# Optimization experiments

Measured on AMD Instinct MI355X. Metric: run time of the kernel, lower is better.

The kernel has to match this reference:

```python
import jax, jax.numpy as jnp
import numpy as np

N, K, D, H = 8192, 32, 128, 256

def setup_inputs() -> dict:
    key = jax.random.key(0)
    ks = jax.random.split(key, 12)
    x = jax.random.normal(ks[0], (N, D), dtype=jnp.float32)
    chosen = jax.random.randint(ks[1], (N, K), 0, N, dtype=jnp.int32)
    # column 0 = the node's own index (matches neighbors[0] == current in the torch code)
    nbrs = jnp.concatenate([jnp.arange(N, dtype=jnp.int32)[:, None], chosen], axis=1)
    t = jax.random.normal(ks[2], (N,), dtype=jnp.float32)
    e_hat = jax.random.normal(ks[3], (N,), dtype=jnp.float32)
    def lin(k, fan_in, fan_out):
        k1, k2 = jax.random.split(k)
        s = 1.0 / np.sqrt(fan_in)
        W = jax.random.uniform(k1, (fan_in, fan_out), minval=-s, maxval=s, dtype=jnp.float32)
        bb = jax.random.uniform(k2, (fan_out,), minval=-s, maxval=s, dtype=jnp.float32)
        return W, bb
    W1, b1 = lin(ks[4], 2 * D, H)
    W2, b2 = lin(ks[5], H, H)
    W3, b3 = lin(ks[6], H, 1)
    b = jnp.float32(1.0)
    return {"x": x, "nbrs": nbrs, "t": t, "e_hat": e_hat,
            "W1": W1, "b1": b1, "W2": W2, "b2": b2, "W3": W3, "b3": b3, "b": b}

def reference(x, nbrs, t, e_hat, W1, b1, W2, b2, W3, b3, b):
    n, d = x.shape
    cur = nbrs[:, 0]          # [n] node's own index
    chosen = nbrs[:, 1:]      # [n, K] neighbor indices
    k = chosen.shape[1]
    z_i = x[cur]              # [n, d]
    z_j = x[chosen]           # [n, K, d] ragged gather (regular degree)
    z_concat = jnp.concatenate(
        [jnp.broadcast_to(z_i[:, None, :], (n, k, d)), z_j], axis=-1)  # [n, K, 2d]
    h = jax.nn.relu(z_concat @ W1 + b1)
    h = jax.nn.relu(h @ W2 + b2)
    mlp_neigh = (h @ W3 + b3)[..., 0]                     # [n, K]
    scores = jax.nn.softmax(b * jnp.abs(mlp_neigh), axis=1)  # per-node softmax
    prop_res = t[chosen] - e_hat[chosen]                  # [n, K]
    w = mlp_neigh * scores                                # [n, K]
    Y_pred = jnp.sum(prop_res * w, axis=1)                # [n]
    pairwise = jnp.zeros((n, n), dtype=x.dtype).at[cur[:, None], chosen].set(w)
    pairwise = pairwise.at[cur, cur].set(0.0)             # zero self-weight last, as in torch
    return Y_pred, pairwise
```

## Files before the change

kernel.cpp:

```cpp
#include <hip/hip_runtime.h>
#include <hip/hip_bf16.h>

typedef short s8v __attribute__((ext_vector_type(8)));
typedef float f4v __attribute__((ext_vector_type(4)));
typedef float f2v __attribute__((ext_vector_type(2)));
typedef unsigned u4v __attribute__((ext_vector_type(4)));

#define NN 8192
#define KN 32
#define DD 128
#define HH 256

static __device__ __forceinline__ unsigned short f2bf(float f) {
    union { float f; unsigned u; } v; v.f = f;
    unsigned r = v.u + 0x7fffu + ((v.u >> 16) & 1u);
    return (unsigned short)(r >> 16);
}
static __device__ __forceinline__ float bf2f(unsigned short h) {
    union { unsigned u; float f; } v; v.u = ((unsigned)h) << 16;
    return v.f;
}
static __device__ __forceinline__ unsigned cvt2(float a, float b) {
    float2 f2; f2.x = a; f2.y = b;
    __hip_bfloat162 h = __float22bfloat162_rn(f2);
    union { __hip_bfloat162 h; unsigned u; } c; c.h = h;
    return c.u;
}
static __device__ __forceinline__ f2v unpk2(unsigned qd) {
    union { unsigned u; float f; } lo, hi;
    lo.u = qd << 16; hi.u = qd & 0xffff0000u;
    f2v r; r[0] = lo.f; r[1] = hi.f; return r;
}

__global__ __launch_bounds__(256) void prep_kernel(
    const float* __restrict__ W1, const float* __restrict__ W2,
    unsigned short* __restrict__ W1sh, unsigned short* __restrict__ W1sl,
    unsigned short* __restrict__ W2s)
{
    int tid = blockIdx.x * 256 + threadIdx.x;
    if (tid < 128 * 512) {
        int k = tid >> 9;
        int n = tid & 511;
        float w = (n < 256) ? W1[k * 256 + n] : W1[(128 + k) * 256 + (n - 256)];
        unsigned short hi = f2bf(w);
        float lo = w - bf2f(hi);
        int idx = ((k >> 5) * 512 + n) * 32 + (k & 31);
        W1sh[idx] = hi;
        W1sl[idx] = f2bf(lo);
    } else {
        int t2 = tid - 128 * 512;
        int k = t2 >> 8;
        int n = t2 & 255;
        W2s[((k >> 5) * 256 + n) * 32 + (k & 31)] = f2bf(W2[k * 256 + n]);
    }
}

__global__ __launch_bounds__(256) void pq_kernel(
    const float* __restrict__ x, const unsigned short* __restrict__ W1sh,
    const unsigned short* __restrict__ W1sl, const float* __restrict__ b1,
    float* __restrict__ P, unsigned short* __restrict__ Q)
{
    __shared__ unsigned short Ah[64 * 136];
    __shared__ unsigned short Al[64 * 136];
    int t  = threadIdx.x;
    int r0 = blockIdx.x * 64;
    int n0 = blockIdx.y * 256;

    {
        int m   = (t & 15) | ((t >> 6) << 4);
        int seg = (t >> 4) & 3;
        const float* xr = x + (r0 + m) * DD + seg * 32;
        #pragma unroll
        for (int it = 0; it < 4; ++it) {
            f4v v0 = *(const f4v*)(xr + it * 8);
            f4v v1 = *(const f4v*)(xr + it * 8 + 4);
            u4v hh, ll;
            #pragma unroll
            for (int pp = 0; pp < 4; ++pp) {
                f2v v;
                v[0] = (pp < 2) ? v0[pp * 2]     : v1[(pp - 2) * 2];
                v[1] = (pp < 2) ? v0[pp * 2 + 1] : v1[(pp - 2) * 2 + 1];
                unsigned hd = cvt2(v[0], v[1]);
                f2v hf = unpk2(hd);
                f2v lo = v - hf;
                hh[pp] = hd;
                ll[pp] = cvt2(lo[0], lo[1]);
            }
            int c = seg * 32 + it * 8;
            *(u4v*)(Ah + m * 136 + c) = hh;
            *(u4v*)(Al + m * 136 + c) = ll;
        }
    }
    __syncthreads();

    int lane = t & 63, wn = t >> 6, l15 = lane & 15, q = lane >> 4;
    f4v acc[4][4];
    #pragma unroll
    for (int mt = 0; mt < 4; ++mt)
        #pragma unroll
        for (int nt = 0; nt < 4; ++nt) acc[mt][nt] = (f4v){0.f, 0.f, 0.f, 0.f};

    #pragma unroll
    for (int kt = 0; kt < 4; ++kt) {
        s8v ah[4], al[4], bh[4], bl[4];
        #pragma unroll
        for (int mt = 0; mt < 4; ++mt) {
            int m = mt * 16 + l15;
            ah[mt] = *(const s8v*)(Ah + m * 136 + kt * 32 + q * 8);
            al[mt] = *(const s8v*)(Al + m * 136 + kt * 32 + q * 8);
        }
        #pragma unroll
        for (int nt = 0; nt < 4; ++nt) {
            int n = n0 + wn * 64 + nt * 16 + l15;
            int idx = (kt * 512 + n) * 32 + q * 8;
            bh[nt] = *(const s8v*)(W1sh + idx);
            bl[nt] = *(const s8v*)(W1sl + idx);
        }
        #pragma unroll
        for (int mt = 0; mt < 4; ++mt)
            #pragma unroll
            for (int nt = 0; nt < 4; ++nt) {
                acc[mt][nt] = __builtin_amdgcn_mfma_f32_16x16x32_bf16(ah[mt], bh[nt], acc[mt][nt], 0, 0, 0);
                acc[mt][nt] = __builtin_amdgcn_mfma_f32_16x16x32_bf16(ah[mt], bl[nt], acc[mt][nt], 0, 0, 0);
                acc[mt][nt] = __builtin_amdgcn_mfma_f32_16x16x32_bf16(al[mt], bh[nt], acc[mt][nt], 0, 0, 0);
            }
    }

    #pragma unroll
    for (int nt = 0; nt < 4; ++nt) {
        int cg = n0 + wn * 64 + nt * 16 + l15;
        if (cg < 256) {
            float bias = b1[cg];
            #pragma unroll
            for (int mt = 0; mt < 4; ++mt)
                #pragma unroll
                for (int r = 0; r < 4; ++r) {
                    int row = r0 + mt * 16 + q * 4 + r;
                    P[row * 256 + cg] = acc[mt][nt][r] + bias;
                }
        } else {
            int cq = cg - 256;
            #pragma unroll
            for (int mt = 0; mt < 4; ++mt)
                #pragma unroll
                for (int r = 0; r < 4; ++r) {
                    int row = r0 + mt * 16 + q * 4 + r;
                    Q[row * 256 + cq] = f2bf(acc[mt][nt][r]);
                }
        }
    }
}

__global__ __launch_bounds__(256) void main_kernel(
    const float* __restrict__ P, const unsigned short* __restrict__ Q,
    const unsigned short* __restrict__ W2s,
    const float* __restrict__ b2, const float* __restrict__ W3,
    const int* __restrict__ nbrs, const float* __restrict__ t_arr,
    const float* __restrict__ e_hat, const float* __restrict__ b3p,
    const float* __restrict__ bscal, float* __restrict__ out)
{
    __shared__ unsigned short A[64 * 264];
    __shared__ float mlpbuf[64][4];
    __shared__ float wbuf_w[2][32];
    __shared__ int   wbuf_j[2][32];
    int t = threadIdx.x;
    int node0 = blockIdx.x * 2;
    float* PW = out + NN;

    {
        int m   = (t & 15) | ((t >> 6) << 4);
        int seg = (t >> 4) & 3;
        int g = node0 + (m >> 5);
        int j = nbrs[g * 33 + 1 + (m & 31)];
        const float* Pr = P + g * 256 + seg * 64;
        const unsigned short* Qr = Q + j * 256 + seg * 64;

        #pragma unroll
        for (int half = 0; half < 2; ++half) {
            f4v p0[4], p1[4];
            u4v qv[4];
            #pragma unroll
            for (int it = 0; it < 4; ++it) {
                int itg = half * 4 + it;
                p0[it] = *(const f4v*)(Pr + itg * 8);
                p1[it] = *(const f4v*)(Pr + itg * 8 + 4);
                qv[it] = *(const u4v*)(Qr + itg * 8);
            }
            #pragma unroll
            for (int it = 0; it < 4; ++it) {
                int itg = half * 4 + it;
                u4v hv;
                #pragma unroll
                for (int pp = 0; pp < 4; ++pp) {
                    f2v pv;
                    pv[0] = (pp < 2) ? p0[it][pp * 2]     : p1[it][(pp - 2) * 2];
                    pv[1] = (pp < 2) ? p0[it][pp * 2 + 1] : p1[it][(pp - 2) * 2 + 1];
                    f2v qf = unpk2(qv[it][pp]);
                    f2v s = pv + qf;
                    s = __builtin_elementwise_max(s, (f2v){0.f, 0.f});
                    hv[pp] = cvt2(s[0], s[1]);
                }
                *(u4v*)(A + m * 264 + seg * 64 + itg * 8) = hv;
            }
        }
    }
    __syncthreads();

    int lane = t & 63, wn = t >> 6, l15 = lane & 15, q = lane >> 4;
    f4v acc[4][4];
    #pragma unroll
    for (int mt = 0; mt < 4; ++mt)
        #pragma unroll
        for (int nt = 0; nt < 4; ++nt) acc[mt][nt] = (f4v){0.f, 0.f, 0.f, 0.f};

    #pragma unroll
    for (int kt = 0; kt < 8; ++kt) {
        s8v a[4], b[4];
        #pragma unroll
        for (int mt = 0; mt < 4; ++mt)
            a[mt] = *(const s8v*)(A + (mt * 16 + l15) * 264 + kt * 32 + q * 8);
        #pragma unroll
        for (int nt = 0; nt < 4; ++nt) {
            int n = wn * 64 + nt * 16 + l15;
            b[nt] = *(const s8v*)(W2s + (kt * 256 + n) * 32 + q * 8);
        }
        #pragma unroll
        for (int mt = 0; mt < 4; ++mt)
            #pragma unroll
            for (int nt = 0; nt < 4; ++nt)
                acc[mt][nt] = __builtin_amdgcn_mfma_f32_16x16x32_bf16(a[mt], b[nt], acc[mt][nt], 0, 0, 0);
    }

    f2v p2[4][2];
    #pragma unroll
    for (int mt = 0; mt < 4; ++mt) {
        p2[mt][0] = (f2v){0.f, 0.f};
        p2[mt][1] = (f2v){0.f, 0.f};
    }
    #pragma unroll
    for (int nt = 0; nt < 4; ++nt) {
        int c = wn * 64 + nt * 16 + l15;
        float bb = b2[c], w3 = W3[c];
        f2v bb2 = (f2v){bb, bb};
        f2v w32 = (f2v){w3, w3};
        #pragma unroll
        for (int mt = 0; mt < 4; ++mt) {
            f2v lo = (f2v){acc[mt][nt][0], acc[mt][nt][1]};
            f2v hi = (f2v){acc[mt][nt][2], acc[mt][nt][3]};
            lo = lo + bb2;
            hi = hi + bb2;
            lo = __builtin_elementwise_max(lo, (f2v){0.f, 0.f});
            hi = __builtin_elementwise_max(hi, (f2v){0.f, 0.f});
            p2[mt][0] = p2[mt][0] + lo * w32;
            p2[mt][1] = p2[mt][1] + hi * w32;
        }
    }
    #pragma unroll
    for (int off = 1; off < 16; off <<= 1)
        #pragma unroll
        for (int mt = 0; mt < 4; ++mt)
            #pragma unroll
            for (int rr = 0; rr < 2; ++rr)
                #pragma unroll
                for (int cc = 0; cc < 2; ++cc)
                    p2[mt][rr][cc] += __shfl_xor(p2[mt][rr][cc], off, 64);
    if (l15 == 0) {
        #pragma unroll
        for (int mt = 0; mt < 4; ++mt)
            #pragma unroll
            for (int r = 0; r < 4; ++r)
                mlpbuf[mt * 16 + q * 4 + r][wn] = p2[mt][r >> 1][r & 1];
    }
    __syncthreads();

    float* img = (float*)A;
    if (t < 128) {
        int node = t >> 6;
        int k = t & 63;
        if (k < 32) {
            int g = node0 + node;
            int m = node * 32 + k;
            float mlp = mlpbuf[m][0] + mlpbuf[m][1] + mlpbuf[m][2] + mlpbuf[m][3] + b3p[0];
            float aabs = bscal[0] * fabsf(mlp);
            float amax = aabs;
            #pragma unroll
            for (int off = 1; off < 32; off <<= 1)
                amax = fmaxf(amax, __shfl_xor(amax, off, 64));
            float e = __expf(aabs - amax);
            float s = e;
            #pragma unroll
            for (int off = 1; off < 32; off <<= 1)
                s += __shfl_xor(s, off, 64);
            float w = mlp * (e / s);

            int j = nbrs[g * 33 + 1 + k];
            float prop = t_arr[j] - e_hat[j];
            float yp = prop * w;
            #pragma unroll
            for (int off = 1; off < 32; off <<= 1)
                yp += __shfl_xor(yp, off, 64);
            if (k == 0) out[g] = yp;

            bool write = (j != g);
            for (int kk = 0; kk < 32; ++kk) {
                int jv = __shfl(j, kk, 64);
                if (kk > k && jv == j) write = false;
            }
            wbuf_w[node][k] = w;
            wbuf_j[node][k] = write ? j : -1;
        }
    } else {
        int tt = t - 128;
        f4v z = (f4v){0.f, 0.f, 0.f, 0.f};
        #pragma unroll
        for (int i = 0; i < 16; ++i)
            *(f4v*)(img + tt * 4 + i * 512) = z;
    }
    __syncthreads();

    if (t < 32) {
        int j = wbuf_j[0][t];
        if (j >= 0) img[j] = wbuf_w[0][t];
    }
    __syncthreads();
    {
        float* dst = PW + (long)node0 * NN;
        f4v z = (f4v){0.f, 0.f, 0.f, 0.f};
        #pragma unroll
        for (int i = 0; i < 8; ++i) {
            f4v v = *(const f4v*)(img + t * 4 + i * 1024);
            *(f4v*)(img + t * 4 + i * 1024) = z;
            __builtin_nontemporal_store(v, (f4v*)(dst + t * 4 + i * 1024));
        }
    }
    __syncthreads();
    if (t < 32) {
        int j = wbuf_j[1][t];
        if (j >= 0) img[j] = wbuf_w[1][t];
    }
    __syncthreads();
    {
        float* dst = PW + (long)(node0 + 1) * NN;
        #pragma unroll
        for (int i = 0; i < 8; ++i) {
            f4v v = *(const f4v*)(img + t * 4 + i * 1024);
            __builtin_nontemporal_store(v, (f4v*)(dst + t * 4 + i * 1024));
        }
    }
}

extern "C" void kernel_launch(void* const* d_in, const int* in_sizes, int n_in,
                              void* d_out, int out_size, void* d_ws, size_t ws_size,
                              hipStream_t stream) {
    const float* x     = (const float*)d_in[0];
    const int*   nbrs  = (const int*)d_in[1];
    const float* t     = (const float*)d_in[2];
    const float* e_hat = (const float*)d_in[3];
    const float* W1    = (const float*)d_in[4];
    const float* b1    = (const float*)d_in[5];
    const float* W2    = (const float*)d_in[6];
    const float* b2    = (const float*)d_in[7];
    const float* W3    = (const float*)d_in[8];
    const float* b3    = (const float*)d_in[9];
    const float* b     = (const float*)d_in[10];

    char* ws = (char*)d_ws;
    float*          P     = (float*)ws;
    unsigned short* Q     = (unsigned short*)(ws + 8388608);
    unsigned short* W1sh  = (unsigned short*)(ws + 12582912);
    unsigned short* W1sl  = (unsigned short*)(ws + 12713984);
    unsigned short* W2s   = (unsigned short*)(ws + 12845056);

    prep_kernel<<<512, 256, 0, stream>>>(W1, W2, W1sh, W1sl, W2s);
    pq_kernel<<<dim3(128, 2), 256, 0, stream>>>(x, W1sh, W1sl, b1, P, Q);
    main_kernel<<<4096, 256, 0, stream>>>(P, Q, W2s, b2, W3, nbrs, t, e_hat,
                                          b3, b, (float*)d_out);
}
```

Baseline: 351.6 us.

## Process one node per 128-thread block instead of two per 256-thread block

Restructures main_kernel so each block handles a single node with 2 waves, each wave computing a 32x128 MFMA tile, and the pairwise row is written in two 4096-column halves through a smaller LDS image. The grid doubles to 8192 blocks and the LDS footprint halves, aiming for more resident blocks and finer-grained scheduling. In exchange, each W2 tile load is shared across fewer rows (32 instead of 64), so W2 traffic per node roughly doubles, and each wave holds more B fragments.

```diff
diff --git a/kernel.cpp b/kernel.cpp
--- a/kernel.cpp
+++ b/kernel.cpp
@@ -151,7 +151,7 @@
     }
 }
 
-__global__ __launch_bounds__(256) void main_kernel(
+__global__ __launch_bounds__(128, 4) void main_kernel(
     const float* __restrict__ P, const unsigned short* __restrict__ Q,
     const unsigned short* __restrict__ W2s,
     const float* __restrict__ b2, const float* __restrict__ W3,
@@ -159,92 +159,80 @@
     const float* __restrict__ e_hat, const float* __restrict__ b3p,
     const float* __restrict__ bscal, float* __restrict__ out)
 {
-    __shared__ unsigned short A[64 * 264];
-    __shared__ float mlpbuf[64][4];
-    __shared__ float wbuf_w[2][32];
-    __shared__ int   wbuf_j[2][32];
+    __shared__ unsigned short A[32 * 264];
+    __shared__ float mlpbuf[32][2];
+    __shared__ float wbuf_w[32];
+    __shared__ int   wbuf_j[32];
     int t = threadIdx.x;
-    int node0 = blockIdx.x * 2;
+    int g = blockIdx.x;
     float* PW = out + NN;
 
     {
         int m   = (t & 15) | ((t >> 6) << 4);
         int seg = (t >> 4) & 3;
-        int g = node0 + (m >> 5);
-        int j = nbrs[g * 33 + 1 + (m & 31)];
+        int j = nbrs[g * 33 + 1 + m];
         const float* Pr = P + g * 256 + seg * 64;
         const unsigned short* Qr = Q + j * 256 + seg * 64;
-
-        #pragma unroll
-        for (int half = 0; half < 2; ++half) {
-            f4v p0[4], p1[4];
-            u4v qv[4];
-            #pragma unroll
-            for (int it = 0; it < 4; ++it) {
-                int itg = half * 4 + it;
-                p0[it] = *(const f4v*)(Pr + itg * 8);
-                p1[it] = *(const f4v*)(Pr + itg * 8 + 4);
-                qv[it] = *(const u4v*)(Qr + itg * 8);
+        #pragma unroll
+        for (int it = 0; it < 8; ++it) {
+            f4v p0 = *(const f4v*)(Pr + it * 8);
+            f4v p1 = *(const f4v*)(Pr + it * 8 + 4);
+            u4v qv = *(const u4v*)(Qr + it * 8);
+            u4v hv;
+            #pragma unroll
+            for (int pp = 0; pp < 4; ++pp) {
+                f2v pv;
+                pv[0] = (pp < 2) ? p0[pp * 2]     : p1[(pp - 2) * 2];
+                pv[1] = (pp < 2) ? p0[pp * 2 + 1] : p1[(pp - 2) * 2 + 1];
+                f2v qf = unpk2(qv[pp]);
+                f2v s = pv + qf;
+                s = __builtin_elementwise_max(s, (f2v){0.f, 0.f});
+                hv[pp] = cvt2(s[0], s[1]);
             }
-            #pragma unroll
-            for (int it = 0; it < 4; ++it) {
-                int itg = half * 4 + it;
-                u4v hv;
-                #pragma unroll
-                for (int pp = 0; pp < 4; ++pp) {
-                    f2v pv;
-                    pv[0] = (pp < 2) ? p0[it][pp * 2]     : p1[it][(pp - 2) * 2];
-                    pv[1] = (pp < 2) ? p0[it][pp * 2 + 1] : p1[it][(pp - 2) * 2 + 1];
-                    f2v qf = unpk2(qv[it][pp]);
-                    f2v s = pv + qf;
-                    s = __builtin_elementwise_max(s, (f2v){0.f, 0.f});
-                    hv[pp] = cvt2(s[0], s[1]);
-                }
-                *(u4v*)(A + m * 264 + seg * 64 + itg * 8) = hv;
-            }
-        }
-    }
-    __syncthreads();
-
-    int lane = t & 63, wn = t >> 6, l15 = lane & 15, q = lane >> 4;
-    f4v acc[4][4];
-    #pragma unroll
-    for (int mt = 0; mt < 4; ++mt)
-        #pragma unroll
-        for (int nt = 0; nt < 4; ++nt) acc[mt][nt] = (f4v){0.f, 0.f, 0.f, 0.f};
+            *(u4v*)(A + m * 264 + seg * 64 + it * 8) = hv;
+        }
+    }
+    __syncthreads();
+
+    int lane = t & 63, w = t >> 6, l15 = lane & 15, q = lane >> 4;
+    f4v acc[2][8];
+    #pragma unroll
+    for (int mt = 0; mt < 2; ++mt)
+        #pragma unroll
+        for (int nt = 0; nt < 8; ++nt) acc[mt][nt] = (f4v){0.f, 0.f, 0.f, 0.f};
 
     #pragma unroll
     for (int kt = 0; kt < 8; ++kt) {
-        s8v a[4], b[4];
-        #pragma unroll
-        for (int mt = 0; mt < 4; ++mt)
+        s8v a[2], b[8];
+        #pragma unroll
+        for (int mt = 0; mt < 2; ++mt)
             a[mt] = *(const s8v*)(A + (mt * 16 + l15) * 264 + kt * 32 + q * 8);
         #pragma unroll
-        for (int nt = 0; nt < 4; ++nt) {
-            int n = wn * 64 + nt * 16 + l15;
+        for (int nt = 0; nt < 8; ++nt) {
+            int n = w * 128 + nt * 16 + l15;
             b[nt] = *(const s8v*)(W2s + (kt * 256 + n) * 32 + q * 8);
         }
         #pragma unroll
-        for (int mt = 0; mt < 4; ++mt)
-            #pragma unroll
-            for (int nt = 0; nt < 4; ++nt)
+        for (int mt = 0; mt < 2; ++mt)
+            #pragma unroll
+            for (int nt = 0; nt < 8; ++nt)
                 acc[mt][nt] = __builtin_amdgcn_mfma_f32_16x16x32_bf16(a[mt], b[nt], acc[mt][nt], 0, 0, 0);
     }
 
-    f2v p2[4][2];
-    #pragma unroll
-    for (int mt = 0; mt < 4; ++mt) {
+    f2v p2[2][2];
+    #pragma unroll
+    for (int mt = 0; mt < 2; ++mt) {
         p2[mt][0] = (f2v){0.f, 0.f};
         p2[mt][1] = (f2v){0.f, 0.f};
     }
     #pragma unroll
-    for (int nt = 0; nt < 4; ++nt) {
-        int c = wn * 64 + nt * 16 + l15;
+    for (int nt = 0; nt < 8; ++nt) {
+        int c = w * 128 + nt * 16 + l15;
         float bb = b2[c], w3 = W3[c];
         f2v bb2 = (f2v){bb, bb};
         f2v w32 = (f2v){w3, w3};
         #pragma unroll
-        for (int mt = 0; mt < 4; ++mt) {
+        for (int mt = 0; mt < 2; ++mt) {
             f2v lo = (f2v){acc[mt][nt][0], acc[mt][nt][1]};
             f2v hi = (f2v){acc[mt][nt][2], acc[mt][nt][3]};
             lo = lo + bb2;
@@ -258,7 +246,7 @@
     #pragma unroll
     for (int off = 1; off < 16; off <<= 1)
         #pragma unroll
-        for (int mt = 0; mt < 4; ++mt)
+        for (int mt = 0; mt < 2; ++mt)
             #pragma unroll
             for (int rr = 0; rr < 2; ++rr)
                 #pragma unroll
@@ -266,85 +254,80 @@
                     p2[mt][rr][cc] += __shfl_xor(p2[mt][rr][cc], off, 64);
     if (l15 == 0) {
         #pragma unroll
-        for (int mt = 0; mt < 4; ++mt)
+        for (int mt = 0; mt < 2; ++mt)
             #pragma unroll
             for (int r = 0; r < 4; ++r)
-                mlpbuf[mt * 16 + q * 4 + r][wn] = p2[mt][r >> 1][r & 1];
+                mlpbuf[mt * 16 + q * 4 + r][w] = p2[mt][r >> 1][r & 1];
     }
     __syncthreads();
 
     float* img = (float*)A;
-    if (t < 128) {
-        int node = t >> 6;
-        int k = t & 63;
-        if (k < 32) {
-            int g = node0 + node;
-            int m = node * 32 + k;
-            float mlp = mlpbuf[m][0] + mlpbuf[m][1] + mlpbuf[m][2] + mlpbuf[m][3] + b3p[0];
-            float aabs = bscal[0] * fabsf(mlp);
-            float amax = aabs;
-            #pragma unroll
-            for (int off = 1; off < 32; off <<= 1)
-                amax = fmaxf(amax, __shfl_xor(amax, off, 64));
-            float e = __expf(aabs - amax);
-            float s = e;
-            #pragma unroll
-            for (int off = 1; off < 32; off <<= 1)
-                s += __shfl_xor(s, off, 64);
-            float w = mlp * (e / s);
-
-            int j = nbrs[g * 33 + 1 + k];
-            float prop = t_arr[j] - e_hat[j];
-            float yp = prop * w;
-            #pragma unroll
-            for (int off = 1; off < 32; off <<= 1)
-                yp += __shfl_xor(yp, off, 64);
-            if (k == 0) out[g] = yp;
-
-            bool write = (j != g);
-            for (int kk = 0; kk < 32; ++kk) {
-                int jv = __shfl(j, kk, 64);
-                if (kk > k && jv == j) write = false;
-            }
-            wbuf_w[node][k] = w;
-            wbuf_j[node][k] = write ? j : -1;
-        }
-    } else {
-        int tt = t - 128;
+    if (t < 32) {
+        int k = t;
+        float mlp = mlpbuf[k][0] + mlpbuf[k][1] + b3p[0];
+        float aabs = bscal[0] * fabsf(mlp);
+        float amax = aabs;
+        #pragma unroll
+        for (int off = 1; off < 32; off <<= 1)
+            amax = fmaxf(amax, __shfl_xor(amax, off, 64));
+        float e = __expf(aabs - amax);
+        float s = e;
+        #pragma unroll
+        for (int off = 1; off < 32; off <<= 1)
+            s += __shfl_xor(s, off, 64);
+        float wv = mlp * (e / s);
+
+        int j = nbrs[g * 33 + 1 + k];
+        float prop = t_arr[j] - e_hat[j];
+        float yp = prop * wv;
+        #pragma unroll
+        for (int off = 1; off < 32; off <<= 1)
+            yp += __shfl_xor(yp, off, 64);
+        if (k == 0) out[g] = yp;
+
+        bool write = (j != g);
+        for (int kk = 0; kk < 32; ++kk) {
+            int jv = __shfl(j, kk, 64);
+            if (kk > k && jv == j) write = false;
+        }
+        wbuf_w[k] = wv;
+        wbuf_j[k] = write ? j : -1;
+    } else if (t >= 64) {
+        int tt = t - 64;
         f4v z = (f4v){0.f, 0.f, 0.f, 0.f};
         #pragma unroll
         for (int i = 0; i < 16; ++i)
-            *(f4v*)(img + tt * 4 + i * 512) = z;
+            *(f4v*)(img + tt * 4 + i * 256) = z;
     }
     __syncthreads();
 
     if (t < 32) {
-        int j = wbuf_j[0][t];
-        if (j >= 0) img[j] = wbuf_w[0][t];
+        int j = wbuf_j[t];
+        if (j >= 0 && j < 4096) img[j] = wbuf_w[t];
     }
     __syncthreads();
     {
-        float* dst = PW + (long)node0 * NN;
+        float* dst = PW + (long)g * NN;
         f4v z = (f4v){0.f, 0.f, 0.f, 0.f};
         #pragma unroll
         for (int i = 0; i < 8; ++i) {
-            f4v v = *(const f4v*)(img + t * 4 + i * 1024);
-            *(f4v*)(img + t * 4 + i * 1024) = z;
-            __builtin_nontemporal_store(v, (f4v*)(dst + t * 4 + i * 1024));
+            f4v v = *(const f4v*)(img + t * 4 + i * 512);
+            *(f4v*)(img + t * 4 + i * 512) = z;
+            __builtin_nontemporal_store(v, (f4v*)(dst + t * 4 + i * 512));
         }
     }
     __syncthreads();
     if (t < 32) {
-        int j = wbuf_j[1][t];
-        if (j >= 0) img[j] = wbuf_w[1][t];
+        int j = wbuf_j[t];
+        if (j >= 4096) img[j - 4096] = wbuf_w[t];
     }
     __syncthreads();
     {
-        float* dst = PW + (long)(node0 + 1) * NN;
+        float* dst = PW + (long)g * NN + 4096;
         #pragma unroll
         for (int i = 0; i < 8; ++i) {
-            f4v v = *(const f4v*)(img + t * 4 + i * 1024);
-            __builtin_nontemporal_store(v, (f4v*)(dst + t * 4 + i * 1024));
+            f4v v = *(const f4v*)(img + t * 4 + i * 512);
+            __builtin_nontemporal_store(v, (f4v*)(dst + t * 4 + i * 512));
         }
     }
 }
@@ -373,6 +356,6 @@
 
     prep_kernel<<<512, 256, 0, stream>>>(W1, W2, W1sh, W1sl, W2s);
     pq_kernel<<<dim3(128, 2), 256, 0, stream>>>(x, W1sh, W1sl, b1, P, Q);
-    main_kernel<<<4096, 256, 0, stream>>>(P, Q, W2s, b2, W3, nbrs, t, e_hat,
+    main_kernel<<<8192, 128, 0, stream>>>(P, Q, W2s, b2, W3, nbrs, t, e_hat,
                                           b3, b, (float*)d_out);
 }
```

Measured after the change: 362.8 us. 1.03x slower.
